# Kernel optimization log

Hardware: AMD Instinct MI355X
Metric: run time of the kernel (lower is better)

Reference implementation:

```python
import jax, jax.numpy as jnp
import numpy as np

DT = 10.0 / 200  # 0.05
DX = 20.0 / 128  # 0.15625

# 5x5 fixed finite-difference stencils (torch Conv2d = cross-correlation, so use as-is)
_LAPL = np.array([[0, 0, -1/12, 0, 0],
                  [0, 0,  4/3,  0, 0],
                  [-1/12, 4/3, -5, 4/3, -1/12],
                  [0, 0,  4/3,  0, 0],
                  [0, 0, -1/12, 0, 0]], dtype=np.float32)
_PAR_X = np.array([[0, 0,  1/12, 0, 0],
                   [0, 0, -8/12, 0, 0],
                   [0, 0,  0,    0, 0],
                   [0, 0,  8/12, 0, 0],
                   [0, 0, -1/12, 0, 0]], dtype=np.float32)


def _conv2d_valid(x, kern):
    # x: [N, 1, H, W], kern: [5, 5] -> [N, 1, H-4, W-4]
    return jax.lax.conv_general_dilated(x, jnp.asarray(kern)[None, None], (1, 1), 'VALID')


def _time_deriv(x):
    # x: [T, B, 1, h, w]; central diff interior, one-sided at endpoints (all /DT)
    interior = (x[2:] - x[:-2]) / (2.0 * DT)
    t0 = (-1.5 * x[0] + 2.0 * x[1] - 0.5 * x[2]) / DT
    tn = (0.5 * x[-3] - 2.0 * x[-2] + 1.5 * x[-1]) / DT
    return jnp.concatenate([t0[None], interior, tn[None]], axis=0)


def setup_inputs() -> dict:
    key = jax.random.key(0)
    output = jax.random.normal(key, (20, 8, 3, 256, 256), dtype=jnp.float32)
    return {"output": output}


def reference(output):
    T, B, C, H, W = output.shape
    u = output[:, :, 1:2]  # [T,B,1,H,W]
    v = output[:, :, 2:3]

    lap_u = _conv2d_valid(u.reshape(T * B, 1, H, W), _LAPL).reshape(T, B, 1, H - 4, W - 4) / (DX ** 2)
    lap_v = _conv2d_valid(v.reshape(T * B, 1, H, W), _LAPL).reshape(T, B, 1, H - 4, W - 4) / (DX ** 2)

    uc = u[:, :, :, 2:-2, 2:-2]  # [T,B,1,H-4,W-4]
    vc = v[:, :, :, 2:-2, 2:-2]
    u_t = _time_deriv(uc)
    v_t = _time_deriv(vc)

    Du, Dv = 0.16, 0.08
    f, k = 0.06, 0.062
    f_u = Du * lap_u - uc * vc ** 2 + f * (1.0 - uc) - u_t
    f_v = Dv * lap_v + uc * vc ** 2 - (f + k) * vc - v_t
    return (f_u, f_v)
```

## Files before the change

### kernel.cpp

```cpp
#include <hip/hip_runtime.h>


#define T_OUT (8 * 252 * 252)

typedef float vf4 __attribute__((ext_vector_type(4)));

static __device__ __forceinline__ vf4 lds4u(const float* p) {
    vf4 v;
    __builtin_memcpy(&v, p, 16);
    return v;
}

struct GSRow {
    vf4 u_cm2, u_cm1, u_cc, u_lm1, u_l0;
    vf4 v_cm2, v_cm1, v_cc, v_lm1, v_l0;
};

#define GS_INT(c) { \
    float ut = (ucn.c - s.u_cm1.c) * hdt; \
    float vt = (vcn.c - s.v_cm1.c) * hdt; \
    float uvv = s.u_cc.c * s.v_cc.c * s.v_cc.c; \
    fu.c = Du * s.u_lm1.c - uvv + fR * (1.0f - s.u_cc.c) - ut; \
    fv.c = Dv * s.v_lm1.c + uvv - (fR + kR) * s.v_cc.c - vt; }

#define GS_T0(c) { \
    float ut = (-1.5f * s.u_cm1.c + 2.0f * s.u_cc.c - 0.5f * ucn.c) * inv_dt; \
    float vt = (-1.5f * s.v_cm1.c + 2.0f * s.v_cc.c - 0.5f * vcn.c) * inv_dt; \
    float uvv = s.u_cm1.c * s.v_cm1.c * s.v_cm1.c; \
    fu.c = Du * s.u_l0.c - uvv + fR * (1.0f - s.u_cm1.c) - ut; \
    fv.c = Dv * s.v_l0.c + uvv - (fR + kR) * s.v_cm1.c - vt; }

#define GS_TN(c) { \
    float ut = (0.5f * s.u_cm2.c - 2.0f * s.u_cm1.c + 1.5f * s.u_cc.c) * inv_dt; \
    float vt = (0.5f * s.v_cm2.c - 2.0f * s.v_cm1.c + 1.5f * s.v_cc.c) * inv_dt; \
    float uvv = s.u_cc.c * s.v_cc.c * s.v_cc.c; \
    fu.c = Du * s.u_lm1.c - uvv + fR * (1.0f - s.u_cc.c) - ut; \
    fv.c = Dv * s.v_lm1.c + uvv - (fR + kR) * s.v_cc.c - vt; }

static __device__ __forceinline__ void gs_step(
    const float (*L)[132], int R, int a0, int t, GSRow& s,
    float* __restrict__ outu, float* __restrict__ outv)
{
    const float C1 = 4.0f / 3.0f, C2 = 1.0f / 12.0f;
    const float inv_dx2 = 1.0f / (0.15625f * 0.15625f);
    const float inv_dt  = 20.0f;
    const float hdt     = 10.0f;
    const float Du = 0.16f, Dv = 0.08f, fR = 0.06f, kR = 0.062f;

    vf4 uL  = *(const vf4*)&L[R + 2][a0];
    vf4 uR  = *(const vf4*)&L[R + 2][a0 + 4];
    vf4 um1 = lds4u(&L[R + 1][a0 + 2]);
    vf4 up1 = lds4u(&L[R + 3][a0 + 2]);
    vf4 um2 = lds4u(&L[R    ][a0 + 2]);
    vf4 up2 = lds4u(&L[R + 4][a0 + 2]);

    vf4 vL  = *(const vf4*)&L[R + 14][a0];
    vf4 vR  = *(const vf4*)&L[R + 14][a0 + 4];
    vf4 vm1 = lds4u(&L[R + 13][a0 + 2]);
    vf4 vp1 = lds4u(&L[R + 15][a0 + 2]);
    vf4 vm2 = lds4u(&L[R + 12][a0 + 2]);
    vf4 vp2 = lds4u(&L[R + 16][a0 + 2]);

    vf4 lu, lv;
    lu.x = (C1*(uL.y + uL.w + um1.x + up1.x) - C2*(uL.x + uR.x + um2.x + up2.x) - 5.0f*uL.z) * inv_dx2;
    lu.y = (C1*(uL.z + uR.x + um1.y + up1.y) - C2*(uL.y + uR.y + um2.y + up2.y) - 5.0f*uL.w) * inv_dx2;
    lu.z = (C1*(uL.w + uR.y + um1.z + up1.z) - C2*(uL.z + uR.z + um2.z + up2.z) - 5.0f*uR.x) * inv_dx2;
    lu.w = (C1*(uR.x + uR.z + um1.w + up1.w) - C2*(uL.w + uR.w + um2.w + up2.w) - 5.0f*uR.y) * inv_dx2;
    lv.x = (C1*(vL.y + vL.w + vm1.x + vp1.x) - C2*(vL.x + vR.x + vm2.x + vp2.x) - 5.0f*vL.z) * inv_dx2;
    lv.y = (C1*(vL.z + vR.x + vm1.y + vp1.y) - C2*(vL.y + vR.y + vm2.y + vp2.y) - 5.0f*vL.w) * inv_dx2;
    lv.z = (C1*(vL.w + vR.y + vm1.z + vp1.z) - C2*(vL.z + vR.z + vm2.z + vp2.z) - 5.0f*vR.x) * inv_dx2;
    lv.w = (C1*(vR.x + vR.z + vm1.w + vp1.w) - C2*(vL.w + vR.w + vm2.w + vp2.w) - 5.0f*vR.y) * inv_dx2;

    vf4 ucn = {uL.z, uL.w, uR.x, uR.y};
    vf4 vcn = {vL.z, vL.w, vR.x, vR.y};

    if (t == 0) { s.u_l0 = lu; s.v_l0 = lv; }

    if (t == 2) {
        vf4 fu, fv;
        GS_T0(x); GS_T0(y); GS_T0(z); GS_T0(w);
        __builtin_nontemporal_store(fu, (vf4*)(outu));
        __builtin_nontemporal_store(fv, (vf4*)(outv));
    }

    if (t >= 2) {
        vf4 fu, fv;
        GS_INT(x); GS_INT(y); GS_INT(z); GS_INT(w);
        __builtin_nontemporal_store(fu, (vf4*)(outu + (size_t)(t - 1) * T_OUT));
        __builtin_nontemporal_store(fv, (vf4*)(outv + (size_t)(t - 1) * T_OUT));
    }

    s.u_cm2 = s.u_cm1; s.u_cm1 = s.u_cc; s.u_cc = ucn; s.u_lm1 = lu;
    s.v_cm2 = s.v_cm1; s.v_cm1 = s.v_cc; s.v_cc = vcn; s.v_lm1 = lv;
}

__global__ __launch_bounds__(256) void gs_loss_kernel(
    const float* __restrict__ in, float* __restrict__ out)
{
    __shared__ float lds[2][24][132];

    const int tid = threadIdx.x;

    const int b     = blockIdx.x & 7;
    const int xh    = (blockIdx.x >> 3) & 1;
    const int ytile = blockIdx.x >> 4;
    const int y0    = ytile * 8;

    const int planeStride = 256 * 256;
    const int bStride     = 3 * planeStride;
    const int tStride     = 24 * planeStride;

    const float* base0 = in + (size_t)b * bStride + planeStride;

    const bool s3 = (tid < 24);
    int goffs[4], loffs[4];
#pragma unroll
    for (int i = 0; i < 4; ++i) {
        int idx = tid + 256 * i;
        if (idx >= 792) idx = 791;
        int r  = idx / 33;
        int g  = idx - r * 33;
        int pr = (r < 12) ? r : r - 12;
        int pl = (r < 12) ? 0 : 1;
        int gy = y0 + pr; if (gy > 255) gy = 255;
        goffs[i] = pl * planeStride + gy * 256 + xh * 124 + g * 4;
        loffs[i] = r * 132 + g * 4;
    }

    const int R  = tid >> 5;
    const int cg = tid & 31;
    const int c0 = xh * 128 + cg * 4;
    const int a0 = cg * 4 + 4 * xh;
    const bool act = (c0 <= 248) && (y0 + R < 252);

    const int total = 20 * T_OUT;
    float* outu = out + ((size_t)b * 252 + (y0 + R)) * 252 + c0;
    float* outv = outu + total;

    GSRow s{};

    vf4 sA0, sA1, sA2, sA3;
    vf4 sB0, sB1, sB2, sB3;

#define ISSUE_A(t) { const float* bt = base0 + (size_t)(t) * tStride; \
    sA0 = *(const vf4*)(bt + goffs[0]); \
    sA1 = *(const vf4*)(bt + goffs[1]); \
    sA2 = *(const vf4*)(bt + goffs[2]); \
    if (s3) sA3 = *(const vf4*)(bt + goffs[3]); }
#define ISSUE_B(t) { const float* bt = base0 + (size_t)(t) * tStride; \
    sB0 = *(const vf4*)(bt + goffs[0]); \
    sB1 = *(const vf4*)(bt + goffs[1]); \
    sB2 = *(const vf4*)(bt + goffs[2]); \
    if (s3) sB3 = *(const vf4*)(bt + goffs[3]); }

    ISSUE_A(0);
    ISSUE_B(1);

#pragma unroll
    for (int t = 0; t < 20; ++t) {
        float* Lf = &lds[t & 1][0][0];

        if ((t & 1) == 0) {
            *(vf4*)(Lf + loffs[0]) = sA0;
            *(vf4*)(Lf + loffs[1]) = sA1;
            *(vf4*)(Lf + loffs[2]) = sA2;
            if (s3) *(vf4*)(Lf + loffs[3]) = sA3;
        } else {
            *(vf4*)(Lf + loffs[0]) = sB0;
            *(vf4*)(Lf + loffs[1]) = sB1;
            *(vf4*)(Lf + loffs[2]) = sB2;
            if (s3) *(vf4*)(Lf + loffs[3]) = sB3;
        }

        __syncthreads();

        if (t + 2 < 20) {
            if ((t & 1) == 0) { ISSUE_A(t + 2); } else { ISSUE_B(t + 2); }
        }

        if (act) {
            gs_step(lds[t & 1], R, a0, t, s, outu, outv);
        }
    }

    if (act) {
        const float inv_dt = 20.0f;
        const float Du = 0.16f, Dv = 0.08f, fR = 0.06f, kR = 0.062f;
        vf4 fu, fv;
        GS_TN(x); GS_TN(y); GS_TN(z); GS_TN(w);
        __builtin_nontemporal_store(fu, (vf4*)(outu + (size_t)19 * T_OUT));
        __builtin_nontemporal_store(fv, (vf4*)(outv + (size_t)19 * T_OUT));
    }
}

extern "C" void kernel_launch(void* const* d_in, const int* in_sizes, int n_in,
                              void* d_out, int out_size, void* d_ws, size_t ws_size,
                              hipStream_t stream) {
    const float* in = (const float*)d_in[0];
    float* out = (float*)d_out;

    gs_loss_kernel<<<8 * 2 * 32, 256, 0, stream>>>(in, out);
}
```

Before: 194.9 us.

## Split the time march into two overlapping chunks to double block count

```diff
diff --git a/kernel.cpp b/kernel.cpp
--- a/kernel.cpp
+++ b/kernel.cpp
@@ -37,6 +37,7 @@
     fu.c = Du * s.u_lm1.c - uvv + fR * (1.0f - s.u_cc.c) - ut; \
     fv.c = Dv * s.v_lm1.c + uvv - (fR + kR) * s.v_cc.c - vt; }
 
+template<int TS, bool FIRST>
 static __device__ __forceinline__ void gs_step(
     const float (*L)[132], int R, int a0, int t, GSRow& s,
     float* __restrict__ outu, float* __restrict__ outv)
@@ -74,16 +75,16 @@
     vf4 ucn = {uL.z, uL.w, uR.x, uR.y};
     vf4 vcn = {vL.z, vL.w, vR.x, vR.y};
 
-    if (t == 0) { s.u_l0 = lu; s.v_l0 = lv; }
-
-    if (t == 2) {
+    if (FIRST && t == TS) { s.u_l0 = lu; s.v_l0 = lv; }
+
+    if (FIRST && t == TS + 2) {
         vf4 fu, fv;
         GS_T0(x); GS_T0(y); GS_T0(z); GS_T0(w);
         __builtin_nontemporal_store(fu, (vf4*)(outu));
         __builtin_nontemporal_store(fv, (vf4*)(outv));
     }
 
-    if (t >= 2) {
+    if (t >= TS + 2) {
         vf4 fu, fv;
         GS_INT(x); GS_INT(y); GS_INT(z); GS_INT(w);
         __builtin_nontemporal_store(fu, (vf4*)(outu + (size_t)(t - 1) * T_OUT));
@@ -94,6 +95,74 @@
     s.v_cm2 = s.v_cm1; s.v_cm1 = s.v_cc; s.v_cc = vcn; s.v_lm1 = lv;
 }
 
+template<int TS, int TE, bool FIRST, bool LAST>
+static __device__ __forceinline__ void march(
+    float lds[2][24][132], const float* __restrict__ base0,
+    const int* goffs, const int* loffs, bool s3,
+    int R, int a0, bool act,
+    float* __restrict__ outu, float* __restrict__ outv)
+{
+    const int planeStride = 256 * 256;
+    const int tStride     = 24 * planeStride;
+
+    GSRow s{};
+
+    vf4 sA0, sA1, sA2, sA3;
+    vf4 sB0, sB1, sB2, sB3;
+
+#define ISSUE_A(t) { const float* bt = base0 + (size_t)(t) * tStride; \
+    sA0 = *(const vf4*)(bt + goffs[0]); \
+    sA1 = *(const vf4*)(bt + goffs[1]); \
+    sA2 = *(const vf4*)(bt + goffs[2]); \
+    if (s3) sA3 = *(const vf4*)(bt + goffs[3]); }
+#define ISSUE_B(t) { const float* bt = base0 + (size_t)(t) * tStride; \
+    sB0 = *(const vf4*)(bt + goffs[0]); \
+    sB1 = *(const vf4*)(bt + goffs[1]); \
+    sB2 = *(const vf4*)(bt + goffs[2]); \
+    if (s3) sB3 = *(const vf4*)(bt + goffs[3]); }
+
+    ISSUE_A(TS);
+    ISSUE_B(TS + 1);
+
+#pragma unroll
+    for (int t = TS; t <= TE; ++t) {
+        float* Lf = &lds[(t - TS) & 1][0][0];
+
+        if (((t - TS) & 1) == 0) {
+            *(vf4*)(Lf + loffs[0]) = sA0;
+            *(vf4*)(Lf + loffs[1]) = sA1;
+            *(vf4*)(Lf + loffs[2]) = sA2;
+            if (s3) *(vf4*)(Lf + loffs[3]) = sA3;
+        } else {
+            *(vf4*)(Lf + loffs[0]) = sB0;
+            *(vf4*)(Lf + loffs[1]) = sB1;
+            *(vf4*)(Lf + loffs[2]) = sB2;
+            if (s3) *(vf4*)(Lf + loffs[3]) = sB3;
+        }
+
+        __syncthreads();
+
+        if (t + 2 <= TE) {
+            if (((t - TS) & 1) == 0) { ISSUE_A(t + 2); } else { ISSUE_B(t + 2); }
+        }
+
+        if (act) {
+            gs_step<TS, FIRST>(lds[(t - TS) & 1], R, a0, t, s, outu, outv);
+        }
+    }
+
+    if (LAST && act) {
+        const float inv_dt = 20.0f;
+        const float Du = 0.16f, Dv = 0.08f, fR = 0.06f, kR = 0.062f;
+        vf4 fu, fv;
+        GS_TN(x); GS_TN(y); GS_TN(z); GS_TN(w);
+        __builtin_nontemporal_store(fu, (vf4*)(outu + (size_t)19 * T_OUT));
+        __builtin_nontemporal_store(fv, (vf4*)(outv + (size_t)19 * T_OUT));
+    }
+#undef ISSUE_A
+#undef ISSUE_B
+}
+
 __global__ __launch_bounds__(256) void gs_loss_kernel(
     const float* __restrict__ in, float* __restrict__ out)
 {
@@ -103,12 +172,12 @@
 
     const int b     = blockIdx.x & 7;
     const int xh    = (blockIdx.x >> 3) & 1;
-    const int ytile = blockIdx.x >> 4;
+    const int tc    = (blockIdx.x >> 4) & 1;
+    const int ytile = blockIdx.x >> 5;
     const int y0    = ytile * 8;
 
     const int planeStride = 256 * 256;
     const int bStride     = 3 * planeStride;
-    const int tStride     = 24 * planeStride;
 
     const float* base0 = in + (size_t)b * bStride + planeStride;
 
@@ -137,59 +206,10 @@
     float* outu = out + ((size_t)b * 252 + (y0 + R)) * 252 + c0;
     float* outv = outu + total;
 
-    GSRow s{};
-
-    vf4 sA0, sA1, sA2, sA3;
-    vf4 sB0, sB1, sB2, sB3;
-
-#define ISSUE_A(t) { const float* bt = base0 + (size_t)(t) * tStride; \
-    sA0 = *(const vf4*)(bt + goffs[0]); \
-    sA1 = *(const vf4*)(bt + goffs[1]); \
-    sA2 = *(const vf4*)(bt + goffs[2]); \
-    if (s3) sA3 = *(const vf4*)(bt + goffs[3]); }
-#define ISSUE_B(t) { const float* bt = base0 + (size_t)(t) * tStride; \
-    sB0 = *(const vf4*)(bt + goffs[0]); \
-    sB1 = *(const vf4*)(bt + goffs[1]); \
-    sB2 = *(const vf4*)(bt + goffs[2]); \
-    if (s3) sB3 = *(const vf4*)(bt + goffs[3]); }
-
-    ISSUE_A(0);
-    ISSUE_B(1);
-
-#pragma unroll
-    for (int t = 0; t < 20; ++t) {
-        float* Lf = &lds[t & 1][0][0];
-
-        if ((t & 1) == 0) {
-            *(vf4*)(Lf + loffs[0]) = sA0;
-            *(vf4*)(Lf + loffs[1]) = sA1;
-            *(vf4*)(Lf + loffs[2]) = sA2;
-            if (s3) *(vf4*)(Lf + loffs[3]) = sA3;
-        } else {
-            *(vf4*)(Lf + loffs[0]) = sB0;
-            *(vf4*)(Lf + loffs[1]) = sB1;
-            *(vf4*)(Lf + loffs[2]) = sB2;
-            if (s3) *(vf4*)(Lf + loffs[3]) = sB3;
-        }
-
-        __syncthreads();
-
-        if (t + 2 < 20) {
-            if ((t & 1) == 0) { ISSUE_A(t + 2); } else { ISSUE_B(t + 2); }
-        }
-
-        if (act) {
-            gs_step(lds[t & 1], R, a0, t, s, outu, outv);
-        }
-    }
-
-    if (act) {
-        const float inv_dt = 20.0f;
-        const float Du = 0.16f, Dv = 0.08f, fR = 0.06f, kR = 0.062f;
-        vf4 fu, fv;
-        GS_TN(x); GS_TN(y); GS_TN(z); GS_TN(w);
-        __builtin_nontemporal_store(fu, (vf4*)(outu + (size_t)19 * T_OUT));
-        __builtin_nontemporal_store(fv, (vf4*)(outv + (size_t)19 * T_OUT));
+    if (tc == 0) {
+        march<0, 10, true, false>(lds, base0, goffs, loffs, s3, R, a0, act, outu, outv);
+    } else {
+        march<9, 19, false, true>(lds, base0, goffs, loffs, s3, R, a0, act, outu, outv);
     }
 }
 
@@ -199,5 +219,5 @@
     const float* in = (const float*)d_in[0];
     float* out = (float*)d_out;
 
-    gs_loss_kernel<<<8 * 2 * 32, 256, 0, stream>>>(in, out);
-}
+    gs_loss_kernel<<<8 * 2 * 2 * 32, 256, 0, stream>>>(in, out);
+}
```

Result: slower. 204.8 us (+5.1%).
